# Performance work log

Measured on AMD Instinct MI355X. Metric: run time of the kernel, lower is better.

## Reference

```python
import jax, jax.numpy as jnp
import numpy as np

N = 16384
IMRATIO = 0.0732
MARGIN = 1.0


def setup_inputs() -> dict:
    key = jax.random.key(0)
    k1, k2 = jax.random.split(key)
    preds = jax.random.normal(k1, (N,), dtype=jnp.float32)
    targets = (jax.random.uniform(k2, (N,)) < IMRATIO).astype(jnp.int32)
    return {"preds": preds, "targets": targets}


def reference(preds, targets):
    # positive = preds[targets==1]; negative = preds[targets==0]
    # loss = mean over P x N pairs of (1 - (p_i - n_j))**2 + margin * relu(1 - (p_i - n_j))
    # Expressed jit-compatibly as a mask-weighted full pairwise reduction (same math).
    pos_w = (targets == 1).astype(preds.dtype)  # [N]
    neg_w = (targets == 0).astype(preds.dtype)  # [N]
    one_minus_diff = 1.0 - (preds[:, None] - preds[None, :])  # [N, N]
    vals = one_minus_diff * one_minus_diff + MARGIN * jax.nn.relu(one_minus_diff)
    w = pos_w[:, None] * neg_w[None, :]  # [N, N] pair indicator
    num_pairs = pos_w.sum() * neg_w.sum()
    return (vals * w).sum() / num_pairs
```

## Files before the change

kernel.cpp:

```cpp
#include <hip/hip_runtime.h>


#define MAXP 4096

__device__ __forceinline__ double wave_reduce_f64(double v) {
    #pragma unroll
    for (int off = 32; off > 0; off >>= 1) v += __shfl_xor(v, off, 64);
    return v;
}

__global__ __launch_bounds__(256)
void aucm_main(const float* __restrict__ preds,
               const int* __restrict__ tgt,
               int n,
               double* __restrict__ reluPart,
               double* __restrict__ moms)
{
    __shared__ __align__(16) float sA[MAXP];
    __shared__ int sWave[4];
    __shared__ double sRed[4][5];

    const int tid   = threadIdx.x;
    const int lane  = tid & 63;
    const int wave  = tid >> 6;
    const int b     = blockIdx.x;
    const int jb    = b & 63;
    const int slice = b >> 6;
    const bool doMom = (b == 0);

    unsigned long long mask = 0ull;
    int c = 0;
    double mA = 0, mA2 = 0, mN = 0, mN2 = 0;
    #pragma unroll
    for (int k = 0; k < 16; ++k) {
        const int base = (tid << 2) + (k << 10);
        const int4 t4 = *reinterpret_cast<const int4*>(&tgt[base]);
        const int f0 = (t4.x == 1), f1 = (t4.y == 1),
                  f2 = (t4.z == 1), f3 = (t4.w == 1);
        mask |= ((unsigned long long)f0 << (k * 4 + 0))
              | ((unsigned long long)f1 << (k * 4 + 1))
              | ((unsigned long long)f2 << (k * 4 + 2))
              | ((unsigned long long)f3 << (k * 4 + 3));
        c += f0 + f1 + f2 + f3;
        if (doMom) {
            const float4 p4 = *reinterpret_cast<const float4*>(&preds[base]);
            const float pv[4] = { p4.x, p4.y, p4.z, p4.w };
            const int   fv[4] = { f0, f1, f2, f3 };
            #pragma unroll
            for (int u = 0; u < 4; ++u) {
                if (fv[u]) { const double a = 1.0 - (double)pv[u]; mA += a; mA2 += a * a; }
                else       { const double p = (double)pv[u];       mN += p; mN2 += p * p; }
            }
        }
    }

    int v = c;
    #pragma unroll
    for (int d = 1; d < 64; d <<= 1) {
        const int t = __shfl_up(v, d, 64);
        if (lane >= d) v += t;
    }
    if (lane == 63) sWave[wave] = v;
    __syncthreads();
    int wOff = 0;
    #pragma unroll
    for (int w = 0; w < 4; ++w) if (w < wave) wOff += sWave[w];
    const int total = sWave[0] + sWave[1] + sWave[2] + sWave[3];
    int g = wOff + v - c;

    const int per  = (total + 3) >> 2;
    const int lo   = slice * per;
    const int hi   = min(total, lo + per);
    const int cntS = max(0, hi - lo);

    if (mask) {
        #pragma unroll
        for (int k = 0; k < 16; ++k) {
            const unsigned gm = (unsigned)((mask >> (k * 4)) & 0xFull);
            if (!gm) continue;
            const int base = (tid << 2) + (k << 10);
            const float4 p4 = *reinterpret_cast<const float4*>(&preds[base]);
            const float pv[4] = { p4.x, p4.y, p4.z, p4.w };
            #pragma unroll
            for (int u = 0; u < 4; ++u) {
                if ((gm >> u) & 1u) {
                    if (g >= lo && g < hi) sA[g - lo] = 1.0f - pv[u];
                    ++g;
                }
            }
        }
    }
    __syncthreads();

    const int j = (jb << 8) + tid;
    double accd = 0.0;
    if (j < n && tgt[j] == 0) {
        const float pj = preds[j];
        int k = 0;
        while (k < cntS) {
            const int end = min(cntS, k + 64);
            float accf = 0.f;
            for (; k + 8 <= end; k += 8) {
                const float4 v0 = *reinterpret_cast<const float4*>(&sA[k]);
                const float4 v1 = *reinterpret_cast<const float4*>(&sA[k + 4]);
                accf += fmaxf(v0.x + pj, 0.f);
                accf += fmaxf(v0.y + pj, 0.f);
                accf += fmaxf(v0.z + pj, 0.f);
                accf += fmaxf(v0.w + pj, 0.f);
                accf += fmaxf(v1.x + pj, 0.f);
                accf += fmaxf(v1.y + pj, 0.f);
                accf += fmaxf(v1.z + pj, 0.f);
                accf += fmaxf(v1.w + pj, 0.f);
            }
            for (; k < end; ++k) accf += fmaxf(sA[k] + pj, 0.f);
            accd += (double)accf;
        }
    }

    double r = wave_reduce_f64(accd);
    if (lane == 0) sRed[wave][0] = r;
    if (doMom) {
        const double rA  = wave_reduce_f64(mA);
        const double rA2 = wave_reduce_f64(mA2);
        const double rN  = wave_reduce_f64(mN);
        const double rN2 = wave_reduce_f64(mN2);
        if (lane == 0) {
            sRed[wave][1] = rA; sRed[wave][2] = rA2;
            sRed[wave][3] = rN; sRed[wave][4] = rN2;
        }
    }
    __syncthreads();
    if (tid == 0) {
        reluPart[b] = sRed[0][0] + sRed[1][0] + sRed[2][0] + sRed[3][0];
        if (doMom) {
            double tA = 0, tA2 = 0, tN = 0, tN2 = 0;
            #pragma unroll
            for (int w = 0; w < 4; ++w) {
                tA += sRed[w][1]; tA2 += sRed[w][2];
                tN += sRed[w][3]; tN2 += sRed[w][4];
            }
            moms[0] = tA; moms[1] = tA2; moms[2] = tN; moms[3] = tN2;
            moms[4] = (double)total;
        }
    }
}

__global__ __launch_bounds__(256)
void aucm_fin(const double* __restrict__ reluPart,
              const double* __restrict__ moms,
              int n, float* __restrict__ out, float margin)
{
    __shared__ double sRed[4];
    const int tid  = threadIdx.x;
    const int lane = tid & 63;
    const int wave = tid >> 6;

    double r = reluPart[tid];
    r = wave_reduce_f64(r);
    if (lane == 0) sRed[wave] = r;
    __syncthreads();
    if (tid == 0) {
        const double tR = sRed[0] + sRed[1] + sRed[2] + sRed[3];
        const double tA  = moms[0], tA2 = moms[1];
        const double tN  = moms[2], tN2 = moms[3];
        const double P   = moms[4];
        const double Nn  = (double)n - P;
        const double sq  = Nn * tA2 + 2.0 * tA * tN + P * tN2;
        out[0] = (float)((sq + (double)margin * tR) / (P * Nn));
    }
}

extern "C" void kernel_launch(void* const* d_in, const int* in_sizes, int n_in,
                              void* d_out, int out_size, void* d_ws, size_t ws_size,
                              hipStream_t stream) {
    const float* preds = (const float*)d_in[0];
    const int*   tgt   = (const int*)d_in[1];
    float* out = (float*)d_out;
    const int n = in_sizes[0];

    char* ws = (char*)d_ws;
    double* reluPart = (double*)(ws + 0);
    double* moms     = (double*)(ws + 2048);

    aucm_main<<<256, 256, 0, stream>>>(preds, tgt, n, reluPart, moms);
    aucm_fin<<<1, 256, 0, stream>>>(reluPart, moms, n, out, 1.0f );
}
```

Before: 75.10 us.

## Tile positives per block to avoid full-array compaction in every block

Each block now loads and compacts only a 1024-element tile of the input instead of scanning all 16384 targets and predictions. The grid grows from 256 to 1024 blocks: 64 negative-column blocks times 16 tiles. Moment sums are computed per tile and reduced in the final kernel. The pair loop also splits its accumulation into two partial sums to shorten the dependency chain. This removes the redundant full-input scan each block did before, at the cost of more blocks, more partial results and a larger final reduction.

```diff
diff --git a/kernel.cpp b/kernel.cpp
--- a/kernel.cpp
+++ b/kernel.cpp
@@ -1,7 +1,9 @@
 #include <hip/hip_runtime.h>
 
 
-#define MAXP 4096
+#define TILE  1024
+#define NTIL  16
+#define NJB   64
 
 __device__ __forceinline__ double wave_reduce_f64(double v) {
     #pragma unroll
@@ -10,49 +12,30 @@
 }
 
 __global__ __launch_bounds__(256)
-void aucm_main(const float* __restrict__ preds,
+void aucm_pair(const float* __restrict__ preds,
                const int* __restrict__ tgt,
                int n,
                double* __restrict__ reluPart,
-               double* __restrict__ moms)
+               double* __restrict__ momPart)
 {
-    __shared__ __align__(16) float sA[MAXP];
-    __shared__ int sWave[4];
-    __shared__ double sRed[4][5];
+    __shared__ __align__(16) float sP[TILE];
+    __shared__ int sWaveC[4];
+    __shared__ double sRed[4][6];
 
-    const int tid   = threadIdx.x;
-    const int lane  = tid & 63;
-    const int wave  = tid >> 6;
-    const int b     = blockIdx.x;
-    const int jb    = b & 63;
-    const int slice = b >> 6;
-    const bool doMom = (b == 0);
+    const int tid  = threadIdx.x;
+    const int lane = tid & 63;
+    const int wave = tid >> 6;
+    const int b    = blockIdx.x;
+    const int jb   = b & (NJB - 1);
+    const int it   = b >> 6;
+    const bool doMom = (jb == 0);
 
-    unsigned long long mask = 0ull;
-    int c = 0;
-    double mA = 0, mA2 = 0, mN = 0, mN2 = 0;
-    #pragma unroll
-    for (int k = 0; k < 16; ++k) {
-        const int base = (tid << 2) + (k << 10);
-        const int4 t4 = *reinterpret_cast<const int4*>(&tgt[base]);
-        const int f0 = (t4.x == 1), f1 = (t4.y == 1),
-                  f2 = (t4.z == 1), f3 = (t4.w == 1);
-        mask |= ((unsigned long long)f0 << (k * 4 + 0))
-              | ((unsigned long long)f1 << (k * 4 + 1))
-              | ((unsigned long long)f2 << (k * 4 + 2))
-              | ((unsigned long long)f3 << (k * 4 + 3));
-        c += f0 + f1 + f2 + f3;
-        if (doMom) {
-            const float4 p4 = *reinterpret_cast<const float4*>(&preds[base]);
-            const float pv[4] = { p4.x, p4.y, p4.z, p4.w };
-            const int   fv[4] = { f0, f1, f2, f3 };
-            #pragma unroll
-            for (int u = 0; u < 4; ++u) {
-                if (fv[u]) { const double a = 1.0 - (double)pv[u]; mA += a; mA2 += a * a; }
-                else       { const double p = (double)pv[u];       mN += p; mN2 += p * p; }
-            }
-        }
-    }
+    const int base = it * TILE + (tid << 2);
+    const int4   t4 = *reinterpret_cast<const int4*>(&tgt[base]);
+    const float4 p4 = *reinterpret_cast<const float4*>(&preds[base]);
+    const int f0 = (t4.x == 1), f1 = (t4.y == 1),
+              f2 = (t4.z == 1), f3 = (t4.w == 1);
+    const int c = f0 + f1 + f2 + f3;
 
     int v = c;
     #pragma unroll
@@ -60,60 +43,54 @@
         const int t = __shfl_up(v, d, 64);
         if (lane >= d) v += t;
     }
-    if (lane == 63) sWave[wave] = v;
+    if (lane == 63) sWaveC[wave] = v;
     __syncthreads();
     int wOff = 0;
     #pragma unroll
-    for (int w = 0; w < 4; ++w) if (w < wave) wOff += sWave[w];
-    const int total = sWave[0] + sWave[1] + sWave[2] + sWave[3];
+    for (int w = 0; w < 4; ++w) if (w < wave) wOff += sWaveC[w];
+    const int cntP = sWaveC[0] + sWaveC[1] + sWaveC[2] + sWaveC[3];
+
     int g = wOff + v - c;
+    if (f0) sP[g++] = 1.0f - p4.x;
+    if (f1) sP[g++] = 1.0f - p4.y;
+    if (f2) sP[g++] = 1.0f - p4.z;
+    if (f3) sP[g++] = 1.0f - p4.w;
 
-    const int per  = (total + 3) >> 2;
-    const int lo   = slice * per;
-    const int hi   = min(total, lo + per);
-    const int cntS = max(0, hi - lo);
-
-    if (mask) {
+    double mA = 0, mA2 = 0, mN = 0, mN2 = 0;
+    if (doMom) {
+        const float pv[4] = { p4.x, p4.y, p4.z, p4.w };
+        const int   fv[4] = { f0, f1, f2, f3 };
         #pragma unroll
-        for (int k = 0; k < 16; ++k) {
-            const unsigned gm = (unsigned)((mask >> (k * 4)) & 0xFull);
-            if (!gm) continue;
-            const int base = (tid << 2) + (k << 10);
-            const float4 p4 = *reinterpret_cast<const float4*>(&preds[base]);
-            const float pv[4] = { p4.x, p4.y, p4.z, p4.w };
-            #pragma unroll
-            for (int u = 0; u < 4; ++u) {
-                if ((gm >> u) & 1u) {
-                    if (g >= lo && g < hi) sA[g - lo] = 1.0f - pv[u];
-                    ++g;
-                }
-            }
+        for (int u = 0; u < 4; ++u) {
+            if (fv[u]) { const double a = 1.0 - (double)pv[u]; mA += a; mA2 += a * a; }
+            else       { const double p = (double)pv[u];       mN += p; mN2 += p * p; }
         }
     }
     __syncthreads();
 
     const int j = (jb << 8) + tid;
     double accd = 0.0;
-    if (j < n && tgt[j] == 0) {
+    if (tgt[j] == 0) {
         const float pj = preds[j];
         int k = 0;
-        while (k < cntS) {
-            const int end = min(cntS, k + 64);
-            float accf = 0.f;
+        while (k < cntP) {
+            const int end = min(cntP, k + 64);
+            float a0 = 0.f, a1 = 0.f;
             for (; k + 8 <= end; k += 8) {
-                const float4 v0 = *reinterpret_cast<const float4*>(&sA[k]);
-                const float4 v1 = *reinterpret_cast<const float4*>(&sA[k + 4]);
-                accf += fmaxf(v0.x + pj, 0.f);
-                accf += fmaxf(v0.y + pj, 0.f);
-                accf += fmaxf(v0.z + pj, 0.f);
-                accf += fmaxf(v0.w + pj, 0.f);
-                accf += fmaxf(v1.x + pj, 0.f);
-                accf += fmaxf(v1.y + pj, 0.f);
-                accf += fmaxf(v1.z + pj, 0.f);
-                accf += fmaxf(v1.w + pj, 0.f);
+                const float4 v0 = *reinterpret_cast<const float4*>(&sP[k]);
+                const float4 v1 = *reinterpret_cast<const float4*>(&sP[k + 4]);
+                a0 += fmaxf(v0.x + pj, 0.f);
+                a1 += fmaxf(v0.y + pj, 0.f);
+                a0 += fmaxf(v0.z + pj, 0.f);
+                a1 += fmaxf(v0.w + pj, 0.f);
+                a0 += fmaxf(v1.x + pj, 0.f);
+                a1 += fmaxf(v1.y + pj, 0.f);
+                a0 += fmaxf(v1.z + pj, 0.f);
+                a1 += fmaxf(v1.w + pj, 0.f);
             }
-            for (; k < end; ++k) accf += fmaxf(sA[k] + pj, 0.f);
-            accd += (double)accf;
+            float at = a0 + a1;
+            for (; k < end; ++k) at += fmaxf(sP[k] + pj, 0.f);
+            accd += (double)at;
         }
     }
 
@@ -139,33 +116,45 @@
                 tA += sRed[w][1]; tA2 += sRed[w][2];
                 tN += sRed[w][3]; tN2 += sRed[w][4];
             }
-            moms[0] = tA; moms[1] = tA2; moms[2] = tN; moms[3] = tN2;
-            moms[4] = (double)total;
+            momPart[it * 8 + 0] = tA;  momPart[it * 8 + 1] = tA2;
+            momPart[it * 8 + 2] = tN;  momPart[it * 8 + 3] = tN2;
+            momPart[it * 8 + 4] = (double)cntP;
         }
     }
 }
 
 __global__ __launch_bounds__(256)
 void aucm_fin(const double* __restrict__ reluPart,
-              const double* __restrict__ moms,
+              const double* __restrict__ momPart,
               int n, float* __restrict__ out, float margin)
 {
-    __shared__ double sRed[4];
+    __shared__ double sRedR[4];
     const int tid  = threadIdx.x;
     const int lane = tid & 63;
     const int wave = tid >> 6;
 
-    double r = reluPart[tid];
+    double r = reluPart[tid] + reluPart[tid + 256]
+             + reluPart[tid + 512] + reluPart[tid + 768];
     r = wave_reduce_f64(r);
-    if (lane == 0) sRed[wave] = r;
+    if (lane == 0) sRedR[wave] = r;
+
+    double mA = 0, mA2 = 0, mN = 0, mN2 = 0, pc = 0;
+    if (tid < NTIL) {
+        mA  = momPart[tid * 8 + 0]; mA2 = momPart[tid * 8 + 1];
+        mN  = momPart[tid * 8 + 2]; mN2 = momPart[tid * 8 + 3];
+        pc  = momPart[tid * 8 + 4];
+    }
+    if (wave == 0) {
+        mA  = wave_reduce_f64(mA);  mA2 = wave_reduce_f64(mA2);
+        mN  = wave_reduce_f64(mN);  mN2 = wave_reduce_f64(mN2);
+        pc  = wave_reduce_f64(pc);
+    }
     __syncthreads();
     if (tid == 0) {
-        const double tR = sRed[0] + sRed[1] + sRed[2] + sRed[3];
-        const double tA  = moms[0], tA2 = moms[1];
-        const double tN  = moms[2], tN2 = moms[3];
-        const double P   = moms[4];
-        const double Nn  = (double)n - P;
-        const double sq  = Nn * tA2 + 2.0 * tA * tN + P * tN2;
+        const double tR = sRedR[0] + sRedR[1] + sRedR[2] + sRedR[3];
+        const double P  = pc;
+        const double Nn = (double)n - P;
+        const double sq = Nn * mA2 + 2.0 * mA * mN + P * mN2;
         out[0] = (float)((sq + (double)margin * tR) / (P * Nn));
     }
 }
@@ -180,8 +169,8 @@
 
     char* ws = (char*)d_ws;
     double* reluPart = (double*)(ws + 0);
-    double* moms     = (double*)(ws + 2048);
+    double* momPart  = (double*)(ws + 8192);
 
-    aucm_main<<<256, 256, 0, stream>>>(preds, tgt, n, reluPart, moms);
-    aucm_fin<<<1, 256, 0, stream>>>(reluPart, moms, n, out, 1.0f );
+    aucm_pair<<<NJB * NTIL, 256, 0, stream>>>(preds, tgt, n, reluPart, momPart);
+    aucm_fin<<<1, 256, 0, stream>>>(reluPart, momPart, n, out, 1.0f );
 }
```

Measured after the change: 62.93 us. 16.2% less time.
